# Kernel optimization log

Hardware: AMD Instinct MI355X
Metric: run time of the kernel (lower is better)

The kernel has to match this reference:

```python
import jax, jax.numpy as jnp
import numpy as np

E = 50000          # number of edges
S = 16             # spherical basis size
KMAX = 16          # max ragged neighbors per edge
K_AVG = 8          # actual neighbors per edge used to build triplets
EMB = 128          # emb_size
INTERM = 64        # emb_size_interm
UNITS_OUT = 128    # units_out


def setup_inputs() -> dict:
    key = jax.random.key(0)
    k1, k2, k3, k4 = jax.random.split(key, 4)
    T = E * K_AVG
    rbf_W1 = jax.random.normal(k1, (E, INTERM, S), dtype=jnp.float32)
    sph = jax.random.normal(k2, (E, S, KMAX), dtype=jnp.float32)
    m = jax.random.normal(k3, (T, EMB), dtype=jnp.float32)
    # he-orthogonal-like init approximated by scaled normal
    weight = jax.random.normal(k4, (EMB, INTERM, UNITS_OUT), dtype=jnp.float32) / np.sqrt(INTERM)
    # collision-free ragged indexing: each edge has K_AVG triplets at slots 0..K_AVG-1
    id_reduce = jnp.repeat(jnp.arange(E, dtype=jnp.int64), K_AVG)
    id_ragged_idx = jnp.tile(jnp.arange(K_AVG, dtype=jnp.int64), E)
    return {"rbf_W1": rbf_W1, "sph": sph, "m": m, "weight": weight,
            "id_reduce": id_reduce, "id_ragged_idx": id_ragged_idx}


def reference(rbf_W1, sph, m, weight, id_reduce, id_ragged_idx):
    E_, S_, Kmax = sph.shape           # Kmax is static from sph's trailing dim
    emb = m.shape[1]
    # scatter-build padded ragged tensor: (E, Kmax, emb)
    m2 = jnp.zeros((E_, Kmax, emb), dtype=m.dtype).at[id_reduce, id_ragged_idx].set(m)
    # sum over ragged neighbors: (E, S, emb)
    sum_k = jnp.matmul(sph, m2)
    # contract spherical basis: (E, interm, emb)
    rbf_W1_sum_k = jnp.matmul(rbf_W1, sum_k)
    # bilinear + channel sum: permute(2,0,1) @ weight, sum over emb channel c
    m_st = jnp.einsum('eic,cio->eo', rbf_W1_sum_k, weight)
    return m_st
```

## Files before the change

### kernel.cpp

```cpp
#include <hip/hip_runtime.h>
#include <hip/hip_bf16.h>


typedef __attribute__((ext_vector_type(8)))  short short8;
typedef __attribute__((ext_vector_type(4)))  short short4v;
typedef __attribute__((ext_vector_type(4)))  float f32x4;
typedef __attribute__((ext_vector_type(16))) float f32x16;
typedef __attribute__((ext_vector_type(4)))  float float4v;

#define S_DIM   16
#define KMAXX   16
#define EMB     128
#define INTERM  64
#define NOUT    128

#define TE      16
#define CB      16
#define NCH     8
#define EPAD    264
#define AC_I    72
#define AC_C    (TE * AC_I + 8)

__device__ __forceinline__ short f2bf(float f) {
    union { float f; unsigned u; } v; v.f = f;
    unsigned r = v.u + 0x7fffu + ((v.u >> 16) & 1u);
    return (short)(r >> 16);
}
__device__ __forceinline__ unsigned pk2(float a, float b) {
    float2 f; f.x = a; f.y = b;
    union { __hip_bfloat162 h; unsigned u; } c;
    c.h = __float22bfloat162_rn(f);
    return c.u;
}
__device__ __forceinline__ short4v pk4(float a, float b, float c, float d) {
    union { unsigned u[2]; short4v s; } r;
    r.u[0] = pk2(a, b); r.u[1] = pk2(c, d);
    return r.s;
}
__device__ __forceinline__ short8 pk8(float4v lo, float4v hi) {
    union { unsigned u[4]; short8 s; } r;
    r.u[0] = pk2(lo[0], lo[1]); r.u[1] = pk2(lo[2], lo[3]);
    r.u[2] = pk2(hi[0], hi[1]); r.u[3] = pk2(hi[2], hi[3]);
    return r.s;
}

__global__ __launch_bounds__(256) void wtrans_kernel(const float* __restrict__ w,
                                                     short* __restrict__ wbf) {
    __shared__ float ws[INTERM * (NOUT + 1)];
    const int c = blockIdx.x;
    const float* wc = w + (long)c * INTERM * NOUT;
    #pragma unroll
    for (int r = 0; r < (INTERM * NOUT) / 256; ++r) {
        int idx = threadIdx.x + r * 256;
        int i = idx >> 7, o = idx & 127;
        ws[i * (NOUT + 1) + o] = wc[idx];
    }
    __syncthreads();
    short* wo = wbf + (long)c * NOUT * INTERM;
    #pragma unroll
    for (int r = 0; r < (INTERM * NOUT) / 256; ++r) {
        int idx = threadIdx.x + r * 256;
        int o = idx >> 6, i = idx & 63;
        wo[idx] = f2bf(ws[i * (NOUT + 1) + o]);
    }
}

__global__ __launch_bounds__(256, 3) void fused_kernel(
    const float* __restrict__ rbf, const float* __restrict__ sph,
    const float* __restrict__ m,   const int* __restrict__ id_reduce,
    const int* __restrict__ id_rag, const short* __restrict__ wbf,
    float* __restrict__ out)
{
    __shared__ __align__(16) short m2t[TE * EPAD];
    __shared__ __align__(16) short swk[TE * 256];
    __shared__ __align__(16) short Ach[CB * AC_C];

    const int tid  = threadIdx.x;
    const int w    = tid >> 6;
    const int lane = tid & 63;
    const int l15  = lane & 15;
    const int q    = lane >> 4;
    const int c31  = lane & 31;
    const int hh   = lane >> 5;
    const int e0   = blockIdx.x * TE;

    for (int i = tid; i < (TE * EPAD) / 2; i += 256) ((int*)m2t)[i] = 0;

    const int trip = tid >> 1;
    const int hf   = tid & 1;
    const long t   = (long)e0 * 8 + trip;
    const int el   = id_reduce[t] - e0;
    const int slot = id_rag[t];
    const bool valid = (el >= 0) && (el < TE) && (slot >= 0) && (slot < KMAXX);
    const int sbase  = el * EPAD + hf * 8 * KMAXX + slot;
    const float* mrow = m + t * EMB + hf * 8;

    short8 sph_fr[4];
    short8 rbf_fr[4][2];
    #pragma unroll
    for (int ee = 0; ee < 4; ++ee) {
        const long ge = e0 + w * 4 + ee;
        if (q < 2) {
            const float* sp = sph + ge * (S_DIM * KMAXX) + l15 * KMAXX + q * 8;
            float4v s0 = *(const float4v*)sp;
            float4v s1 = *(const float4v*)(sp + 4);
            sph_fr[ee] = pk8(s0, s1);
        } else {
            sph_fr[ee] = (short8){0,0,0,0,0,0,0,0};
        }
        #pragma unroll
        for (int it = 0; it < 2; ++it) {
            const float* rp = rbf + ge * (INTERM * S_DIM) + (it * 32 + c31) * S_DIM + hh * 8;
            float4v r0 = *(const float4v*)rp;
            float4v r1 = *(const float4v*)(rp + 4);
            rbf_fr[ee][it] = pk8(r0, r1);
        }
    }

    float4v mc0 = *(const float4v*)(mrow);
    float4v mc1 = *(const float4v*)(mrow + 4);

    f32x4 acc0 = {0.f,0.f,0.f,0.f}, acc1 = {0.f,0.f,0.f,0.f};

    __syncthreads();

    for (int ch = 0; ch < NCH; ++ch) {
        if (valid) {
            #pragma unroll
            for (int jj = 0; jj < 4; ++jj)
                m2t[sbase + jj * KMAXX] = f2bf(mc0[jj]);
            #pragma unroll
            for (int jj = 0; jj < 4; ++jj)
                m2t[sbase + (jj + 4) * KMAXX] = f2bf(mc1[jj]);
        }
        __syncthreads();

        #pragma unroll
        for (int ee = 0; ee < 4; ++ee) {
            const int e = w * 4 + ee;
            short8 bf = (q < 2) ? *(const short8*)&m2t[e * EPAD + l15 * KMAXX + q * 8]
                                : (short8){0,0,0,0,0,0,0,0};
            f32x4 d1 = {0.f,0.f,0.f,0.f};
            d1 = __builtin_amdgcn_mfma_f32_16x16x32_bf16(sph_fr[ee], bf, d1, 0, 0, 0);
            *(short4v*)&swk[e * 256 + l15 * 16 + q * 4] = pk4(d1[0], d1[1], d1[2], d1[3]);
        }
        #pragma unroll
        for (int ee = 0; ee < 4; ++ee) {
            const int e = w * 4 + ee;
            short8 bfr = (c31 < 16) ? *(const short8*)&swk[e * 256 + c31 * 16 + hh * 8]
                                    : (short8){0,0,0,0,0,0,0,0};
            #pragma unroll
            for (int it = 0; it < 2; ++it) {
                f32x16 d2 = {0.f,0.f,0.f,0.f,0.f,0.f,0.f,0.f,
                             0.f,0.f,0.f,0.f,0.f,0.f,0.f,0.f};
                d2 = __builtin_amdgcn_mfma_f32_32x32x16_bf16(rbf_fr[ee][it], bfr, d2, 0, 0, 0);
                if (c31 < 16) {
                    #pragma unroll
                    for (int rg = 0; rg < 4; ++rg) {
                        const int i0 = it * 32 + rg * 8 + hh * 4;
                        *(short4v*)&Ach[c31 * AC_C + e * AC_I + i0] =
                            pk4(d2[rg*4], d2[rg*4+1], d2[rg*4+2], d2[rg*4+3]);
                    }
                }
            }
        }
        __syncthreads();

        const int chn = (ch + 1) & 7;
        float4v mn0 = *(const float4v*)(mrow + chn * CB);
        float4v mn1 = *(const float4v*)(mrow + chn * CB + 4);

        #pragma unroll 4
        for (int cc = 0; cc < CB; ++cc) {
            short8 a0 = *(const short8*)&Ach[cc * AC_C + l15 * AC_I + q * 8];
            short8 a1 = *(const short8*)&Ach[cc * AC_C + l15 * AC_I + 32 + q * 8];
            const int c = ch * CB + cc;
            const short* wp0 = wbf + ((long)c * NOUT + (w * 2 + 0) * 16 + l15) * INTERM + q * 8;
            const short* wp1 = wbf + ((long)c * NOUT + (w * 2 + 1) * 16 + l15) * INTERM + q * 8;
            acc0 = __builtin_amdgcn_mfma_f32_16x16x32_bf16(a0, *(const short8*)wp0,        acc0, 0, 0, 0);
            acc0 = __builtin_amdgcn_mfma_f32_16x16x32_bf16(a1, *(const short8*)(wp0 + 32), acc0, 0, 0, 0);
            acc1 = __builtin_amdgcn_mfma_f32_16x16x32_bf16(a0, *(const short8*)wp1,        acc1, 0, 0, 0);
            acc1 = __builtin_amdgcn_mfma_f32_16x16x32_bf16(a1, *(const short8*)(wp1 + 32), acc1, 0, 0, 0);
        }
        __syncthreads();

        mc0 = mn0; mc1 = mn1;
    }

    #pragma unroll
    for (int r = 0; r < 4; ++r) {
        out[(long)(e0 + q * 4 + r) * NOUT + w * 32 + l15]      = acc0[r];
        out[(long)(e0 + q * 4 + r) * NOUT + w * 32 + 16 + l15] = acc1[r];
    }
}

extern "C" void kernel_launch(void* const* d_in, const int* in_sizes, int n_in,
                              void* d_out, int out_size, void* d_ws, size_t ws_size,
                              hipStream_t stream) {
    const float* rbf = (const float*)d_in[0];
    const float* sph = (const float*)d_in[1];
    const float* m   = (const float*)d_in[2];
    const float* w   = (const float*)d_in[3];
    const int* idr   = (const int*)d_in[4];
    const int* idg   = (const int*)d_in[5];
    float* out       = (float*)d_out;
    short* wbf       = (short*)d_ws;

    const int E = in_sizes[1] / (S_DIM * KMAXX);

    hipLaunchKernelGGL(wtrans_kernel, dim3(EMB), dim3(256), 0, stream, w, wbf);
    hipLaunchKernelGGL(fused_kernel, dim3(E / TE), dim3(256), 0, stream,
                       rbf, sph, m, idr, idg, wbf, out);
}
```

Before: 1.139 ms.

## Halve channel block, raise occupancy, drop a barrier per chunk, use nontemporal I/O

Cuts the channel block from 16 to 8. This halves the LDS staging buffers, so launch bounds can rise from 3 to 5 blocks per CU. It also reorders the loop so the next chunk's ragged m tile is written right after the mid barrier, removing one __syncthreads per chunk, with m prefetched two chunks ahead. rbf/sph loads and output stores become nontemporal. The trade-off is that the stage-1 and stage-2 MFMAs now run twice as often with half of their N columns idle, which wastes matrix throughput.

```diff
diff --git a/kernel.cpp b/kernel.cpp
--- a/kernel.cpp
+++ b/kernel.cpp
@@ -15,9 +15,10 @@
 #define NOUT    128
 
 #define TE      16
-#define CB      16
-#define NCH     8
-#define EPAD    264
+#define CB      8
+#define NCH     (EMB / CB)
+#define EPAD    (CB * KMAXX + 8)
+#define SWS     (CB * 16)
 #define AC_I    72
 #define AC_C    (TE * AC_I + 8)
 
@@ -43,6 +44,9 @@
     r.u[2] = pk2(hi[0], hi[1]); r.u[3] = pk2(hi[2], hi[3]);
     return r.s;
 }
+__device__ __forceinline__ float4v ntl4(const float* p) {
+    return __builtin_nontemporal_load((const float4v*)p);
+}
 
 __global__ __launch_bounds__(256) void wtrans_kernel(const float* __restrict__ w,
                                                      short* __restrict__ wbf) {
@@ -65,14 +69,14 @@
     }
 }
 
-__global__ __launch_bounds__(256, 3) void fused_kernel(
+__global__ __launch_bounds__(256, 5) void fused_kernel(
     const float* __restrict__ rbf, const float* __restrict__ sph,
     const float* __restrict__ m,   const int* __restrict__ id_reduce,
     const int* __restrict__ id_rag, const short* __restrict__ wbf,
     float* __restrict__ out)
 {
     __shared__ __align__(16) short m2t[TE * EPAD];
-    __shared__ __align__(16) short swk[TE * 256];
+    __shared__ __align__(16) short swk[TE * SWS];
     __shared__ __align__(16) short Ach[CB * AC_C];
 
     const int tid  = threadIdx.x;
@@ -92,8 +96,8 @@
     const int el   = id_reduce[t] - e0;
     const int slot = id_rag[t];
     const bool valid = (el >= 0) && (el < TE) && (slot >= 0) && (slot < KMAXX);
-    const int sbase  = el * EPAD + hf * 8 * KMAXX + slot;
-    const float* mrow = m + t * EMB + hf * 8;
+    const int sbase  = el * EPAD + hf * 4 * KMAXX + slot;
+    const float* mrow = m + t * EMB + hf * 4;
 
     short8 sph_fr[4];
     short8 rbf_fr[4][2];
@@ -102,8 +106,8 @@
         const long ge = e0 + w * 4 + ee;
         if (q < 2) {
             const float* sp = sph + ge * (S_DIM * KMAXX) + l15 * KMAXX + q * 8;
-            float4v s0 = *(const float4v*)sp;
-            float4v s1 = *(const float4v*)(sp + 4);
+            float4v s0 = ntl4(sp);
+            float4v s1 = ntl4(sp + 4);
             sph_fr[ee] = pk8(s0, s1);
         } else {
             sph_fr[ee] = (short8){0,0,0,0,0,0,0,0};
@@ -111,50 +115,48 @@
         #pragma unroll
         for (int it = 0; it < 2; ++it) {
             const float* rp = rbf + ge * (INTERM * S_DIM) + (it * 32 + c31) * S_DIM + hh * 8;
-            float4v r0 = *(const float4v*)rp;
-            float4v r1 = *(const float4v*)(rp + 4);
+            float4v r0 = ntl4(rp);
+            float4v r1 = ntl4(rp + 4);
             rbf_fr[ee][it] = pk8(r0, r1);
         }
     }
 
-    float4v mc0 = *(const float4v*)(mrow);
-    float4v mc1 = *(const float4v*)(mrow + 4);
-
     f32x4 acc0 = {0.f,0.f,0.f,0.f}, acc1 = {0.f,0.f,0.f,0.f};
 
+    float4v mc = *(const float4v*)(mrow);
     __syncthreads();
+    if (valid) {
+        #pragma unroll
+        for (int jj = 0; jj < 4; ++jj)
+            m2t[sbase + jj * KMAXX] = f2bf(mc[jj]);
+    }
+    mc = *(const float4v*)(mrow + CB);
 
     for (int ch = 0; ch < NCH; ++ch) {
-        if (valid) {
-            #pragma unroll
-            for (int jj = 0; jj < 4; ++jj)
-                m2t[sbase + jj * KMAXX] = f2bf(mc0[jj]);
-            #pragma unroll
-            for (int jj = 0; jj < 4; ++jj)
-                m2t[sbase + (jj + 4) * KMAXX] = f2bf(mc1[jj]);
-        }
         __syncthreads();
 
         #pragma unroll
         for (int ee = 0; ee < 4; ++ee) {
             const int e = w * 4 + ee;
-            short8 bf = (q < 2) ? *(const short8*)&m2t[e * EPAD + l15 * KMAXX + q * 8]
-                                : (short8){0,0,0,0,0,0,0,0};
+            short8 bf = (q < 2 && l15 < CB)
+                      ? *(const short8*)&m2t[e * EPAD + l15 * KMAXX + q * 8]
+                      : (short8){0,0,0,0,0,0,0,0};
             f32x4 d1 = {0.f,0.f,0.f,0.f};
             d1 = __builtin_amdgcn_mfma_f32_16x16x32_bf16(sph_fr[ee], bf, d1, 0, 0, 0);
-            *(short4v*)&swk[e * 256 + l15 * 16 + q * 4] = pk4(d1[0], d1[1], d1[2], d1[3]);
+            if (l15 < CB)
+                *(short4v*)&swk[e * SWS + l15 * 16 + q * 4] = pk4(d1[0], d1[1], d1[2], d1[3]);
         }
         #pragma unroll
         for (int ee = 0; ee < 4; ++ee) {
             const int e = w * 4 + ee;
-            short8 bfr = (c31 < 16) ? *(const short8*)&swk[e * 256 + c31 * 16 + hh * 8]
+            short8 bfr = (c31 < CB) ? *(const short8*)&swk[e * SWS + c31 * 16 + hh * 8]
                                     : (short8){0,0,0,0,0,0,0,0};
             #pragma unroll
             for (int it = 0; it < 2; ++it) {
                 f32x16 d2 = {0.f,0.f,0.f,0.f,0.f,0.f,0.f,0.f,
                              0.f,0.f,0.f,0.f,0.f,0.f,0.f,0.f};
                 d2 = __builtin_amdgcn_mfma_f32_32x32x16_bf16(rbf_fr[ee][it], bfr, d2, 0, 0, 0);
-                if (c31 < 16) {
+                if (c31 < CB) {
                     #pragma unroll
                     for (int rg = 0; rg < 4; ++rg) {
                         const int i0 = it * 32 + rg * 8 + hh * 4;
@@ -166,9 +168,12 @@
         }
         __syncthreads();
 
-        const int chn = (ch + 1) & 7;
-        float4v mn0 = *(const float4v*)(mrow + chn * CB);
-        float4v mn1 = *(const float4v*)(mrow + chn * CB + 4);
+        if (valid) {
+            #pragma unroll
+            for (int jj = 0; jj < 4; ++jj)
+                m2t[sbase + jj * KMAXX] = f2bf(mc[jj]);
+        }
+        float4v mn = *(const float4v*)(mrow + ((ch + 2) & (NCH - 1)) * CB);
 
         #pragma unroll 4
         for (int cc = 0; cc < CB; ++cc) {
@@ -182,15 +187,13 @@
             acc1 = __builtin_amdgcn_mfma_f32_16x16x32_bf16(a0, *(const short8*)wp1,        acc1, 0, 0, 0);
             acc1 = __builtin_amdgcn_mfma_f32_16x16x32_bf16(a1, *(const short8*)(wp1 + 32), acc1, 0, 0, 0);
         }
-        __syncthreads();
-
-        mc0 = mn0; mc1 = mn1;
+        mc = mn;
     }
 
     #pragma unroll
     for (int r = 0; r < 4; ++r) {
-        out[(long)(e0 + q * 4 + r) * NOUT + w * 32 + l15]      = acc0[r];
-        out[(long)(e0 + q * 4 + r) * NOUT + w * 32 + 16 + l15] = acc1[r];
+        __builtin_nontemporal_store(acc0[r], &out[(long)(e0 + q * 4 + r) * NOUT + w * 32 + l15]);
+        __builtin_nontemporal_store(acc1[r], &out[(long)(e0 + q * 4 + r) * NOUT + w * 32 + 16 + l15]);
     }
 }
 
```

After: 1.262 ms. 1.11x slower.
